# Performance work log

Hardware: AMD Instinct MI355X
Metric: run time of the kernel (lower is better)

## Reference

```python
import jax, jax.numpy as jnp
import numpy as np

# --- SLAYER params (nmnistNet.yaml) ---
THETA = 10.0
TS = 1.0
TAU_REF = 1.0
SCALE_REF = 2.0
T_SAMPLE = 300
B = 8

def _alpha_kernel(tau, mult, t_sample, ts, eps=0.01):
    vals = []
    t = 0.0
    while t < t_sample:
        v = mult * t / tau * np.exp(1.0 - t / tau)
        if abs(v) < eps and t > tau:
            break
        vals.append(v)
        t += ts
    return np.asarray(vals, np.float32)

# refractory kernel: alpha kernel with mult = -scaleRef*theta (slayer._calculateRefKernel)
REF_KERNEL = _alpha_kernel(TAU_REF, -SCALE_REF * THETA, T_SAMPLE, TS)
NREF = REF_KERNEL.shape[0]  # 11 for these params; REF_KERNEL[0] == 0


def spike(u):
    """slayerCuda.getSpikes: per-neuron sequential threshold recurrence over time.
    u: [..., T] membrane potential. On spike at t, REF_KERNEL is accumulated
    into u[t:t+NREF]; spike amplitude is 1/Ts."""
    uT = jnp.moveaxis(u, -1, 0)  # [T, ...]
    refk = jnp.asarray(REF_KERNEL[1:]).reshape((NREF - 1,) + (1,) * (u.ndim - 1))
    buf0 = jnp.zeros((NREF - 1,) + uT.shape[1:], u.dtype)  # pending refractory

    def step(buf, u_t):
        u_mod = u_t + buf[0]
        ev = (u_mod >= THETA).astype(u.dtype)
        buf = jnp.concatenate([buf[1:], jnp.zeros_like(buf[:1])], axis=0) + ev[None] * refk
        return buf, ev / TS

    _, s = jax.lax.scan(step, buf0, uT)
    return jnp.moveaxis(s, 0, -1)


def conv2d_t(x, w, pad):
    """slayer.conv: Conv3d with kernel (k,k,1) == per-timestep 2D conv.
    x: [B,C,H,W,T], w: [O,I,kh,kw]."""
    b, c, h, wd, t = x.shape
    xb = jnp.moveaxis(x, -1, 1).reshape(b * t, c, h, wd)
    y = jax.lax.conv_general_dilated(xb, w, (1, 1), [(pad, pad), (pad, pad)],
                                     dimension_numbers=('NCHW', 'OIHW', 'NCHW'))
    o, ho, wo = y.shape[1], y.shape[2], y.shape[3]
    return jnp.moveaxis(y.reshape(b, t, o, ho, wo), 1, -1)


def sum_pool2(x):
    """slayer.pool(2): fixed-weight (1.1*theta) 2x2/stride-2 sum over H,W per channel."""
    y = jax.lax.reduce_window(x, 0.0, jax.lax.add, (1, 1, 2, 2, 1), (1, 1, 2, 2, 1), 'VALID')
    return 1.1 * THETA * y


def setup_inputs():
    key = jax.random.key(0)
    k0, k1, k2, k3, k4 = jax.random.split(key, 5)
    spikeInput = (jax.random.uniform(k0, (B, 2, 34, 34, T_SAMPLE)) < 0.1).astype(jnp.float32) / TS
    # conv weights: kaiming-uniform bound * 100 (the __init__ scales conv weights by 100)
    w1 = jax.random.uniform(k1, (16, 2, 5, 5), minval=-14.1, maxval=14.1, dtype=jnp.float32)
    w2 = jax.random.uniform(k2, (32, 16, 3, 3), minval=-8.3, maxval=8.3, dtype=jnp.float32)
    w3 = jax.random.uniform(k3, (64, 32, 3, 3), minval=-5.9, maxval=5.9, dtype=jnp.float32)
    wfc = jax.random.uniform(k4, (10, 64, 8, 8), minval=-0.5, maxval=0.5, dtype=jnp.float32)
    return {"spikeInput": spikeInput, "w1": w1, "w2": w2, "w3": w3, "wfc": wfc}


def reference(spikeInput, w1, w2, w3, wfc):
    s1 = spike(conv2d_t(spikeInput, w1, 1))  # [B,16,32,32,T]
    s2 = spike(sum_pool2(s1))                # [B,16,16,16,T]
    s3 = spike(conv2d_t(s2, w2, 1))          # [B,32,16,16,T]
    s4 = spike(sum_pool2(s3))                # [B,32,8,8,T]
    s5 = spike(conv2d_t(s4, w3, 1))          # [B,64,8,8,T]
    # dense((8,8,64),10): Conv3d(64,10,(8,8,1)) == full-spatial contraction
    u = jnp.einsum('bchwt,ochw->bot', s5, wfc)[:, :, None, None, :]
    return spike(u)                          # [B,10,1,1,T]
```

## Files before the change

kernel.cpp:

```cpp
#include <hip/hip_runtime.h>
#include <hip/hip_bf16.h>
#include <cmath>

#define T_SAMPLE 300
#define NCHUNK 75

typedef __attribute__((ext_vector_type(8))) short short8;
typedef __attribute__((ext_vector_type(4))) float f32x4;

struct RefK { float v[10]; };

__device__ __forceinline__ unsigned char spike_step(float u, float* buf, const RefK& rk) {
    const float um = u + buf[0];
    const bool fire = um >= 10.0f;
    const float ev = fire ? 1.0f : 0.0f;
#pragma unroll
    for (int r = 0; r < 9; ++r) buf[r] = fmaf(ev, rk.v[r], buf[r + 1]);
    buf[9] = ev * rk.v[9];
    return fire ? (unsigned char)1 : (unsigned char)0;
}

__device__ __forceinline__ short8 bytes_to_bf16x8(uint2 w8) {
    union { uint4 u; short8 s8; } cv;
    cv.u.x = (w8.x & 0xFFu) * 0x3F80u | ((((w8.x >> 8) & 0xFFu) * 0x3F80u) << 16);
    cv.u.y = ((w8.x >> 16) & 0xFFu) * 0x3F80u | ((((w8.x >> 24) & 0xFFu) * 0x3F80u) << 16);
    cv.u.z = (w8.y & 0xFFu) * 0x3F80u | ((((w8.y >> 8) & 0xFFu) * 0x3F80u) << 16);
    cv.u.w = ((w8.y >> 16) & 0xFFu) * 0x3F80u | ((((w8.y >> 24) & 0xFFu) * 0x3F80u) << 16);
    return cv.s8;
}

__device__ __forceinline__ unsigned short bf16_split_sel(float w, int s) {
    __hip_bfloat16 hb = __float2bfloat16(w);
    const float hf = __bfloat162float(hb);
    __hip_bfloat16 mb = __float2bfloat16(w - hf);
    const float mf = __bfloat162float(mb);
    __hip_bfloat16 lb = __float2bfloat16(w - hf - mf);
    __hip_bfloat16 sel = (s == 0) ? hb : ((s == 1) ? mb : lb);
    return *(unsigned short*)&sel;
}

__global__ __launch_bounds__(256) void transpose_in_k(
    const float* __restrict__ In, unsigned int* __restrict__ X)
{
    __shared__ unsigned int lds[16 * NCHUNK];
    const int blk = blockIdx.x;
    const int tn = threadIdx.x >> 4;
    const int tq = threadIdx.x & 15;
    const size_t n = (size_t)blk * 16 + tn;
#pragma unroll
    for (int p = 0; p < 5; ++p) {
        const int ch = p * 16 + tq;
        if (ch < NCHUNK) {
            const float4 v = *(const float4*)(In + n * T_SAMPLE + ch * 4);
            unsigned int u = (v.x != 0.f ? 1u : 0u) | (v.y != 0.f ? 0x100u : 0u) |
                             (v.z != 0.f ? 0x10000u : 0u) | (v.w != 0.f ? 0x1000000u : 0u);
            lds[tn * NCHUNK + ch] = u;
        }
    }
    __syncthreads();
    for (int idx = threadIdx.x; idx < 16 * NCHUNK; idx += 256) {
        const int ch = idx >> 4, t2 = idx & 15;
        X[(size_t)ch * 18496 + blk * 16 + t2] = lds[t2 * NCHUNK + ch];
    }
}

__global__ __launch_bounds__(256) void prep_w1_k(
    const float* __restrict__ w1, unsigned short* __restrict__ Wr1)
{
    const int g = blockIdx.x * 256 + threadIdx.x;
    const int j = g & 7;
    const int lane = (g >> 3) & 63;
    const int ks = (g >> 9) & 3;
    const int s = g >> 11;
    const int q = lane >> 4;
    const int oc = lane & 15;
    const int kg = ks * 32 + q * 8 + j;
    const int slot = kg >> 2, c = kg & 1;
    const int dy = slot / 6, dx = slot % 6;
    const float w = (dy < 5 && dx < 5) ? w1[((oc * 2 + c) * 5 + dy) * 5 + dx] * 0.5f : 0.f;
    Wr1[g] = bf16_split_sel(w, s);
}

__global__ __launch_bounds__(256) void prep_w3_k(
    const float* __restrict__ w3, unsigned short* __restrict__ Wr)
{
    const int g = blockIdx.x * 256 + threadIdx.x;
    const int j = g & 7;
    const int lane = (g >> 3) & 63;
    const int mt = (g >> 9) & 3;
    const int rest = g >> 11;
    const int ks = rest % 9;
    const int s = rest / 9;
    const int oc = mt * 16 + (lane & 15);
    const int ic = (lane >> 4) * 8 + j;
    Wr[g] = bf16_split_sel(w3[(oc * 32 + ic) * 9 + ks], s);
}

__global__ __launch_bounds__(256) void prep_w2_k(
    const float* __restrict__ w2, unsigned short* __restrict__ Wr2)
{
    const int g = blockIdx.x * 256 + threadIdx.x;
    const int j = g & 7;
    const int lane = (g >> 3) & 63;
    const int mt = (g >> 9) & 1;
    const int rest = g >> 10;
    const int kp = rest % 5;
    const int s = rest / 5;
    const int q = lane >> 4;
    const int oc = mt * 16 + (lane & 15);
    const int tap = kp * 2 + (q >> 1);
    const int ic = (q & 1) * 8 + j;
    const float w = (tap <= 8) ? w2[(oc * 16 + ic) * 9 + tap] : 0.f;
    Wr2[g] = bf16_split_sel(w, s);
}

__device__ __forceinline__ void c1_mfma_chunk(
    const unsigned int* __restrict__ tb, const int* offA, const int* offB,
    const short8* Af, f32x4* acc)
{
    unsigned int vA[4][4], vB[4][4];
#pragma unroll
    for (int ks = 0; ks < 4; ++ks)
#pragma unroll
        for (int t = 0; t < 4; ++t) {
            vA[ks][t] = tb[t * 72 + offA[ks]];
            vB[ks][t] = tb[t * 72 + offB[ks]];
        }

#pragma unroll
    for (int t = 0; t < 4; ++t) acc[t] = (f32x4){0.f, 0.f, 0.f, 0.f};
#pragma unroll
    for (int ks = 0; ks < 4; ++ks)
#pragma unroll
        for (int t = 0; t < 4; ++t) {
            union { uint4 u; short8 s8; } cv;
            cv.u.x = vA[ks][t]; cv.u.y = vA[ks][t];
            cv.u.z = vB[ks][t]; cv.u.w = vB[ks][t];
#pragma unroll
            for (int s = 0; s < 3; ++s)
                acc[t] = __builtin_amdgcn_mfma_f32_16x16x32_bf16(
                    Af[s * 4 + ks], cv.s8, acc[t], 0, 0, 0);
        }
}

__global__ __launch_bounds__(512, 4) void conv1pc_k(
    const unsigned int* __restrict__ X, const unsigned short* __restrict__ Wr1,
    uchar4* __restrict__ S1, RefK rk)
{
    __shared__ unsigned int tab[2][4 * 288];
    __shared__ __align__(16) float4 Ulds[2][4 * 256];
    const int pg = blockIdx.x;
    const int b = blockIdx.y;
    const int ty = pg >> 2, tx = pg & 3;
    const int tid = threadIdx.x;
    const int wv = tid >> 6, lane = tid & 63;
    const bool isConv = (wv >= 4);
    const int q = lane >> 4, n = lane & 15;
    const int py0 = n >> 3, px0 = n & 7;

    short8 Af[12];
    int offA[4], offB[4];
    int lidx[2], gof[2];
    unsigned int w0[2], w1[2];
    if (isConv) {
#pragma unroll
        for (int s = 0; s < 3; ++s)
#pragma unroll
            for (int ks = 0; ks < 4; ++ks)
                Af[s * 4 + ks] = *(const short8*)(Wr1 + (((s * 4 + ks) * 64 + lane) * 8));
#pragma unroll
        for (int ks = 0; ks < 4; ++ks) {
            const int sA = ks * 8 + q * 2, sB = sA + 1;
            const int dyA = sA / 6, dxA = sA - dyA * 6;
            const int dyB = sB / 6, dxB = sB - dyB * 6;
            offA[ks] = min(py0 + dyA, 5) * 12 + min(px0 + dxA, 11);
            offB[ks] = min(py0 + dyB, 5) * 12 + min(px0 + dxB, 11);
        }
        const int tid2 = tid - 256;
#pragma unroll
        for (int i = 0; i < 2; ++i) {
            const int e = i * 256 + tid2;
            if (e < 288) {
                const int chl = e / 72, site = e - chl * 72;
                const int r = site / 12, cc = site - r * 12;
                const int gy = ty * 2 - 1 + r, gx = tx * 8 - 1 + cc;
                lidx[i] = chl * 288 + site;
                gof[i] = (((unsigned)gy < 34u) && ((unsigned)gx < 34u))
                       ? (chl * 18496 + (b * 2) * 1156 + gy * 34 + gx) : -1;
            } else { lidx[i] = -1; gof[i] = -1; }
        }
#pragma unroll
        for (int i = 0; i < 2; ++i) {
            if (gof[i] >= 0) { w0[i] = X[gof[i]]; w1[i] = X[gof[i] + 1156]; }
            else { w0[i] = 0u; w1[i] = 0u; }
        }
#pragma unroll
        for (int i = 0; i < 2; ++i) {
            if (lidx[i] >= 0) {
#pragma unroll
                for (int t = 0; t < 4; ++t)
                    tab[0][lidx[i] + t * 72] =
                        ((w0[i] >> (8 * t)) & 0xFFu) * 0x3F80u
                        | ((((w1[i] >> (8 * t)) & 0xFFu) * 0x3F80u) << 16);
            }
        }
    }

    float buf[10];
#pragma unroll
    for (int r = 0; r < 10; ++r) buf[r] = 0.f;
    const int s_oc = (tid & 255) >> 4, s_n = tid & 15;
    const int nb0 = (b * 16 + s_oc) * 1024 + (ty * 2 + (s_n >> 3)) * 32 + tx * 8 + (s_n & 7);

    __syncthreads();

    for (int w = 0; w < 19; ++w) {
        const int cb = w & 1;
        if (isConv) {
            if (w < 18) {
                const unsigned int* Xs = X + (size_t)(w + 1) * (4 * 18496);
#pragma unroll
                for (int i = 0; i < 2; ++i) {
                    if (gof[i] >= 0) { w0[i] = Xs[gof[i]]; w1[i] = Xs[gof[i] + 1156]; }
                }
            }
            const int CW = (w == 18) ? 3 : 4;
            const int k = wv - 4;
            if (k < CW) {
                f32x4 acc[4];
                c1_mfma_chunk(&tab[cb][k * 288], offA, offB, Af, acc);
#pragma unroll
                for (int rr = 0; rr < 4; ++rr)
                    Ulds[cb][k * 256 + (q * 4 + rr) * 16 + n] =
                        make_float4(acc[0][rr], acc[1][rr], acc[2][rr], acc[3][rr]);
            }
            if (w < 18) {
#pragma unroll
                for (int i = 0; i < 2; ++i) {
                    if (lidx[i] >= 0) {
#pragma unroll
                        for (int t = 0; t < 4; ++t)
                            tab[cb ^ 1][lidx[i] + t * 72] =
                                ((w0[i] >> (8 * t)) & 0xFFu) * 0x3F80u
                                | ((((w1[i] >> (8 * t)) & 0xFFu) * 0x3F80u) << 16);
                    }
                }
            }
        } else if (w > 0) {
            const int pb = (w - 1) & 1;
            for (int k = 0; k < 4; ++k) {
                const float4 u = Ulds[pb][k * 256 + tid];
                uchar4 o;
                o.x = spike_step(u.x, buf, rk);
                o.y = spike_step(u.y, buf, rk);
                o.z = spike_step(u.z, buf, rk);
                o.w = spike_step(u.w, buf, rk);
                S1[(size_t)((w - 1) * 4 + k) * 131072 + nb0] = o;
            }
        }
        __syncthreads();
    }
    if (!isConv) {
        for (int k = 0; k < 3; ++k) {
            const float4 u = Ulds[0][k * 256 + tid];
            uchar4 o;
            o.x = spike_step(u.x, buf, rk);
            o.y = spike_step(u.y, buf, rk);
            o.z = spike_step(u.z, buf, rk);
            o.w = spike_step(u.w, buf, rk);
            S1[(size_t)(72 + k) * 131072 + nb0] = o;
        }
    }
}

__global__ __launch_bounds__(256) void conv2_mfma_k(
    const unsigned int* __restrict__ s2u, const unsigned short* __restrict__ Wr2,
    float4* __restrict__ U, int b0, int nbl)
{
    __shared__ __align__(16) unsigned char pad[4 * 18 * 18 * 16];
    const int tc = blockIdx.x;
    const int bl = blockIdx.z;
    const int b = b0 + bl;
    const int tid = threadIdx.x;
    const int wv = tid >> 6, lane = tid & 63;
    const int q = lane >> 4, n = lane & 15;
    const int PLANE_U = nbl * 8192;

    unsigned int* lp = (unsigned int*)pad;
    for (int i = tid; i < 5184; i += 256) lp[i] = 0u;
    __syncthreads();
    const unsigned int* sb = s2u + (size_t)tc * 32768 + b * 4096;
    for (int e = tid; e < 4096; e += 256) {
        const unsigned int v = sb[e];
        const int c = e >> 8, pix = e & 255;
        const int base = (((pix >> 4) + 1) * 18 + ((pix & 15) + 1)) * 16 + c;
        pad[base]         = (unsigned char)(v & 0xFFu);
        pad[5184 + base]  = (unsigned char)((v >> 8) & 0xFFu);
        pad[10368 + base] = (unsigned char)((v >> 16) & 0xFFu);
        pad[15552 + base] = (unsigned char)(v >> 24);
    }
    __syncthreads();

    for (int i = 0; i < 4; ++i) {
        const int r = wv * 4 + i;
        f32x4 acc[2][4];
#pragma unroll
        for (int mt = 0; mt < 2; ++mt)
#pragma unroll
            for (int t = 0; t < 4; ++t) acc[mt][t] = (f32x4){0.f, 0.f, 0.f, 0.f};

        for (int kp = 0; kp < 5; ++kp) {
            short8 Af[6];
#pragma unroll
            for (int s = 0; s < 3; ++s)
#pragma unroll
                for (int mt = 0; mt < 2; ++mt)
                    Af[s * 2 + mt] = *(const short8*)(Wr2 + ((((s * 5 + kp) * 2 + mt) * 64 + lane) * 8));
            int tap = kp * 2 + (q >> 1);
            if (tap > 8) tap = 8;
            const int dy = tap / 3, dx = tap % 3;
#pragma unroll
            for (int t = 0; t < 4; ++t) {
                const int off = ((t * 18 + r + dy) * 18 + (n + dx)) * 16 + (q & 1) * 8;
                const short8 Bf = bytes_to_bf16x8(*(const uint2*)(pad + off));
#pragma unroll
                for (int s = 0; s < 3; ++s)
#pragma unroll
                    for (int mt = 0; mt < 2; ++mt)
                        acc[mt][t] = __builtin_amdgcn_mfma_f32_16x16x32_bf16(
                            Af[s * 2 + mt], Bf, acc[mt][t], 0, 0, 0);
            }
        }

        const size_t ub = (size_t)tc * PLANE_U;
#pragma unroll
        for (int mt = 0; mt < 2; ++mt)
#pragma unroll
            for (int rr = 0; rr < 4; ++rr) {
                const int oc = mt * 16 + q * 4 + rr;
                const int nb = (bl * 32 + oc) * 256 + r * 16 + n;
                U[ub + nb] = make_float4(acc[mt][0][rr], acc[mt][1][rr], acc[mt][2][rr], acc[mt][3][rr]);
            }
    }
}

__global__ __launch_bounds__(256) void conv3_mfma_k(
    const unsigned int* __restrict__ s4u, const unsigned short* __restrict__ Wr,
    float4* __restrict__ U)
{
    __shared__ __align__(16) unsigned char pad[12800];
    const int tc = blockIdx.x;
    const int bl = blockIdx.z;
    const int tid = threadIdx.x;
    const int wv = tid >> 6, lane = tid & 63;
    const int q = lane >> 4, n = lane & 15;

    unsigned int* lp = (unsigned int*)pad;
    for (int i = tid; i < 3200; i += 256) lp[i] = 0u;
    __syncthreads();
    const unsigned int* sb = s4u + (size_t)tc * 16384 + bl * 2048;
    for (int e = tid; e < 2048; e += 256) {
        const unsigned int v = sb[e];
        const int c = e >> 6, pix = e & 63;
        const int base = (((pix >> 3) + 1) * 10 + ((pix & 7) + 1)) * 32 + c;
        pad[base]        = (unsigned char)(v & 0xFFu);
        pad[3200 + base] = (unsigned char)((v >> 8) & 0xFFu);
        pad[6400 + base] = (unsigned char)((v >> 16) & 0xFFu);
        pad[9600 + base] = (unsigned char)(v >> 24);
    }
    __syncthreads();

    const int pixel = wv * 16 + n;
    const int py0 = pixel >> 3, px0 = pixel & 7;

    f32x4 acc[4][4];
#pragma unroll
    for (int mt = 0; mt < 4; ++mt)
#pragma unroll
        for (int t = 0; t < 4; ++t) acc[mt][t] = (f32x4){0.f, 0.f, 0.f, 0.f};

    for (int ks = 0; ks < 9; ++ks) {
        const int dy = ks / 3, dx = ks % 3;
        short8 Af[12];
#pragma unroll
        for (int s = 0; s < 3; ++s)
#pragma unroll
            for (int mt = 0; mt < 4; ++mt)
                Af[s * 4 + mt] = *(const short8*)(Wr + ((((s * 9 + ks) * 4 + mt) * 64 + lane) * 8));
#pragma unroll
        for (int t = 0; t < 4; ++t) {
            const int off = ((t * 10 + py0 + dy) * 10 + (px0 + dx)) * 32 + q * 8;
            const short8 Bf = bytes_to_bf16x8(*(const uint2*)(pad + off));
#pragma unroll
            for (int s = 0; s < 3; ++s)
#pragma unroll
                for (int mt = 0; mt < 4; ++mt)
                    acc[mt][t] = __builtin_amdgcn_mfma_f32_16x16x32_bf16(
                        Af[s * 4 + mt], Bf, acc[mt][t], 0, 0, 0);
        }
    }

    const size_t ub = (size_t)tc * 32768 + (size_t)bl * 4096;
#pragma unroll
    for (int mt = 0; mt < 4; ++mt)
#pragma unroll
        for (int r = 0; r < 4; ++r) {
            const int oc = mt * 16 + q * 4 + r;
            const int nb = oc * 64 + wv * 16 + n;
            U[ub + nb] = make_float4(acc[mt][0][r], acc[mt][1][r], acc[mt][2][r], acc[mt][3][r]);
        }
}

__device__ __forceinline__ void spike_body(
    const float4* __restrict__ U, uchar4* __restrict__ S,
    int nneur, int sstride, int soff, const RefK& rk)
{
    const int n = blockIdx.x * 64 + threadIdx.x;
    const float4* up = U + n;
    uchar4* sp = S + soff + n;
    float buf[10];
#pragma unroll
    for (int r = 0; r < 10; ++r) buf[r] = 0.f;

    float4 ring[8];
#pragma unroll
    for (int r = 0; r < 8; ++r) ring[r] = up[(size_t)r * nneur];

#pragma unroll 8
    for (int ch = 0; ch < 72; ++ch) {
        const float4 cur = ring[ch & 7];
        const int pf = (ch + 8 < NCHUNK) ? ch + 8 : NCHUNK - 1;
        ring[ch & 7] = up[(size_t)pf * nneur];
        uchar4 o;
        o.x = spike_step(cur.x, buf, rk);
        o.y = spike_step(cur.y, buf, rk);
        o.z = spike_step(cur.z, buf, rk);
        o.w = spike_step(cur.w, buf, rk);
        sp[(size_t)ch * sstride] = o;
    }
#pragma unroll
    for (int ch = 72; ch < NCHUNK; ++ch) {
        const float4 cur = ring[ch & 7];
        uchar4 o;
        o.x = spike_step(cur.x, buf, rk);
        o.y = spike_step(cur.y, buf, rk);
        o.z = spike_step(cur.z, buf, rk);
        o.w = spike_step(cur.w, buf, rk);
        sp[(size_t)ch * sstride] = o;
    }
}

__global__ __launch_bounds__(64) void spike2_k(
    const float4* U, uchar4* S, int nneur, int sstride, int soff, RefK rk)
{ spike_body(U, S, nneur, sstride, soff, rk); }

__global__ __launch_bounds__(64) void spike3_k(
    const float4* U, uchar4* S, int nneur, int sstride, int soff, RefK rk)
{ spike_body(U, S, nneur, sstride, soff, rk); }

__device__ __forceinline__ int bsum4(uint2 r0, uint2 r1, int k) {
    return (int)((r0.x >> (8 * k)) & 0xffu) + (int)((r0.y >> (8 * k)) & 0xffu)
         + (int)((r1.x >> (8 * k)) & 0xffu) + (int)((r1.y >> (8 * k)) & 0xffu);
}

template <int C, int H, int W>
__device__ __forceinline__ void pool_body(
    const uchar4* __restrict__ Sin, uchar4* __restrict__ Sout, const RefK& rk)
{
    constexpr int H2 = H / 2, W2 = W / 2;
    constexpr int SIN = 8 * C * H * W;
    constexpr int SOUT = 8 * C * H2 * W2;
    const int n = blockIdx.x * 64 + threadIdx.x;
    const int x = n % W2;
    const int y = (n / W2) % H2;
    const int c = (n / (W2 * H2)) % C;
    const int b = n / (W2 * H2 * C);
    const int base = (((b * C + c) * H + 2 * y) * W + 2 * x);
    uchar4* q = Sout + n;

    float buf[10];
#pragma unroll
    for (int r = 0; r < 10; ++r) buf[r] = 0.f;

    uint2 r0[8], r1[8];
#pragma unroll
    for (int r = 0; r < 8; ++r) {
        r0[r] = *(const uint2*)(Sin + (size_t)r * SIN + base);
        r1[r] = *(const uint2*)(Sin + (size_t)r * SIN + base + W);
    }

#pragma unroll 8
    for (int ch = 0; ch < 72; ++ch) {
        const uint2 a0 = r0[ch & 7], a1 = r1[ch & 7];
        const int pf = (ch + 8 < NCHUNK) ? ch + 8 : NCHUNK - 1;
        r0[ch & 7] = *(const uint2*)(Sin + (size_t)pf * SIN + base);
        r1[ch & 7] = *(const uint2*)(Sin + (size_t)pf * SIN + base + W);
        uchar4 o;
        o.x = spike_step(11.0f * (float)bsum4(a0, a1, 0), buf, rk);
        o.y = spike_step(11.0f * (float)bsum4(a0, a1, 1), buf, rk);
        o.z = spike_step(11.0f * (float)bsum4(a0, a1, 2), buf, rk);
        o.w = spike_step(11.0f * (float)bsum4(a0, a1, 3), buf, rk);
        q[(size_t)ch * SOUT] = o;
    }
#pragma unroll
    for (int ch = 72; ch < NCHUNK; ++ch) {
        const uint2 a0 = r0[ch & 7], a1 = r1[ch & 7];
        uchar4 o;
        o.x = spike_step(11.0f * (float)bsum4(a0, a1, 0), buf, rk);
        o.y = spike_step(11.0f * (float)bsum4(a0, a1, 1), buf, rk);
        o.z = spike_step(11.0f * (float)bsum4(a0, a1, 2), buf, rk);
        o.w = spike_step(11.0f * (float)bsum4(a0, a1, 3), buf, rk);
        q[(size_t)ch * SOUT] = o;
    }
}

__global__ __launch_bounds__(64) void pool2_k(
    const uchar4* Sin, uchar4* Sout, RefK rk) { pool_body<16, 32, 32>(Sin, Sout, rk); }
__global__ __launch_bounds__(64) void pool4_k(
    const uchar4* Sin, uchar4* Sout, RefK rk) { pool_body<32, 16, 16>(Sin, Sout, rk); }

__global__ __launch_bounds__(64) void dense_k(
    const uchar4* __restrict__ S5, const float* __restrict__ WFC,
    float4* __restrict__ U6)
{
    const int tc = blockIdx.x, o = blockIdx.y, b = blockIdx.z;
    const int lane = threadIdx.x;
    float a0 = 0.f, a1 = 0.f, a2 = 0.f, a3 = 0.f;
    const uchar4* sb = S5 + (size_t)tc * 32768 + b * 4096;
    const float* wb = WFC + o * 4096;
    for (int i = 0; i < 64; ++i) {
        const int site = i * 64 + lane;
        const uchar4 s = sb[site];
        const float w = wb[site];
        a0 = fmaf(w, (float)s.x, a0);
        a1 = fmaf(w, (float)s.y, a1);
        a2 = fmaf(w, (float)s.z, a2);
        a3 = fmaf(w, (float)s.w, a3);
    }
#pragma unroll
    for (int m = 1; m < 64; m <<= 1) {
        a0 += __shfl_xor(a0, m, 64);
        a1 += __shfl_xor(a1, m, 64);
        a2 += __shfl_xor(a2, m, 64);
        a3 += __shfl_xor(a3, m, 64);
    }
    if (lane == 0)
        U6[(size_t)tc * 80 + b * 10 + o] = make_float4(a0, a1, a2, a3);
}

__global__ __launch_bounds__(128) void spike6_k(
    const float4* __restrict__ U6, float* __restrict__ Out, RefK rk)
{
    const int n = threadIdx.x;
    if (n >= 80) return;
    const float4* up = U6 + n;
    float* op = Out + (size_t)n * T_SAMPLE;
    float buf[10];
#pragma unroll
    for (int r = 0; r < 10; ++r) buf[r] = 0.f;

    float4 ring[8];
#pragma unroll
    for (int r = 0; r < 8; ++r) ring[r] = up[(size_t)r * 80];

#pragma unroll 8
    for (int ch = 0; ch < 72; ++ch) {
        const float4 cur = ring[ch & 7];
        const int pf = (ch + 8 < NCHUNK) ? ch + 8 : NCHUNK - 1;
        ring[ch & 7] = up[(size_t)pf * 80];
        float4 o;
        o.x = (float)spike_step(cur.x, buf, rk);
        o.y = (float)spike_step(cur.y, buf, rk);
        o.z = (float)spike_step(cur.z, buf, rk);
        o.w = (float)spike_step(cur.w, buf, rk);
        *(float4*)(op + ch * 4) = o;
    }
#pragma unroll
    for (int ch = 72; ch < NCHUNK; ++ch) {
        const float4 cur = ring[ch & 7];
        float4 o;
        o.x = (float)spike_step(cur.x, buf, rk);
        o.y = (float)spike_step(cur.y, buf, rk);
        o.z = (float)spike_step(cur.z, buf, rk);
        o.w = (float)spike_step(cur.w, buf, rk);
        *(float4*)(op + ch * 4) = o;
    }
}

extern "C" void kernel_launch(void* const* d_in, const int* in_sizes, int n_in,
                              void* d_out, int out_size, void* d_ws, size_t ws_size,
                              hipStream_t stream)
{
    const float* spikeIn = (const float*)d_in[0];
    const float* w1 = (const float*)d_in[1];
    const float* w2 = (const float*)d_in[2];
    const float* w3 = (const float*)d_in[3];
    const float* wfc = (const float*)d_in[4];
    float* out = (float*)d_out;

    RefK rk;
    for (int t = 1; t <= 10; ++t)
        rk.v[t - 1] = (float)(-20.0 * (double)t * std::exp(1.0 - (double)t));

    const size_t A_BYTES = 39321600;
    const size_t B_BYTES = 9830400;
    const size_t U6_BYTES = 96000;
    const size_t U_BIG = 78643200, U_SMALL = 39321600;
    const size_t TAIL = A_BYTES + B_BYTES + U6_BYTES;
    const bool big = ws_size >= U_BIG + TAIL;
    const size_t U_BYTES = big ? U_BIG : U_SMALL;

    char* ws = (char*)d_ws;
    float4* U = (float4*)ws;
    uchar4* A = (uchar4*)(ws + U_BYTES);
    uchar4* Bb = (uchar4*)(ws + U_BYTES + A_BYTES);
    float4* U6 = (float4*)(ws + U_BYTES + A_BYTES + B_BYTES);
    unsigned short* Wr = (unsigned short*)(ws + U_BYTES + 20971520);
    unsigned short* Wr2 = (unsigned short*)(ws + U_BYTES + 20971520 + 131072);
    unsigned short* Wr1 = (unsigned short*)(ws + U_BYTES + A_BYTES + 5570560);

    uchar4* X = Bb;
    uchar4* s1 = A;
    uchar4* s2 = Bb;
    uchar4* s3 = A;
    uchar4* s4 = Bb;
    uchar4* s5 = A;

    transpose_in_k<<<18496 / 16, 256, 0, stream>>>(spikeIn, (unsigned int*)X);
    prep_w1_k<<<24, 256, 0, stream>>>(w1, Wr1);

    {
        dim3 g1(64, 8);
        conv1pc_k<<<g1, 512, 0, stream>>>((const unsigned int*)X, Wr1, s1, rk);
    }
    pool2_k<<<32768 / 64, 64, 0, stream>>>(s1, s2, rk);
    prep_w2_k<<<60, 256, 0, stream>>>(w2, Wr2);
    prep_w3_k<<<216, 256, 0, stream>>>(w3, Wr);
    const int nbl2 = big ? 8 : 4;
    for (int b0 = 0; b0 < 8; b0 += nbl2) {
        dim3 g2(NCHUNK, 1, nbl2);
        conv2_mfma_k<<<g2, 256, 0, stream>>>((const unsigned int*)s2, Wr2, U, b0, nbl2);
        const int nn = nbl2 * 8192;
        spike2_k<<<nn / 64, 64, 0, stream>>>(U, s3, nn, 65536, b0 * 8192, rk);
    }
    pool4_k<<<16384 / 64, 64, 0, stream>>>(s3, s4, rk);
    {
        dim3 g3(NCHUNK, 1, 8);
        conv3_mfma_k<<<g3, 256, 0, stream>>>((const unsigned int*)s4, Wr, U);
        spike3_k<<<32768 / 64, 64, 0, stream>>>(U, s5, 32768, 32768, 0, rk);
    }
    {
        dim3 g6(NCHUNK, 10, 8);
        dense_k<<<g6, 64, 0, stream>>>(s5, wfc, U6);
    }
    spike6_k<<<1, 128, 0, stream>>>(U6, out, rk);
}
```

Before: 249.4 us.

## Fuse first pooling-spike stage into conv1 kernel via shared-memory spike buffer

Adds a ninth wavefront to the conv1 block that consumes the layer-1 spikes from shared memory, does the 2x2 sum-pool and the second spike recurrence, and writes pooled spikes directly. This removes the global write and re-read of the full s1 tensor and the separate pool2 kernel launch. The pool runs one stage behind the spike wavefronts and adds an extra LDS buffer. The single pool wave does sequential work per chunk, which may lengthen the critical path, and dropping the (512,4) occupancy hint may lower occupancy.

```diff
diff --git a/kernel.cpp b/kernel.cpp
--- a/kernel.cpp
+++ b/kernel.cpp
@@ -143,18 +143,33 @@
         }
 }
 
-__global__ __launch_bounds__(512, 4) void conv1pc_k(
+__device__ __forceinline__ uchar4 pool_step4(
+    unsigned int g0, unsigned int g1, unsigned int g2, unsigned int g3,
+    float* buf2, const RefK& rk)
+{
+    uchar4 po;
+    po.x = spike_step(11.0f * (float)(((g0 >> 0) & 0xff) + ((g1 >> 0) & 0xff) + ((g2 >> 0) & 0xff) + ((g3 >> 0) & 0xff)), buf2, rk);
+    po.y = spike_step(11.0f * (float)(((g0 >> 8) & 0xff) + ((g1 >> 8) & 0xff) + ((g2 >> 8) & 0xff) + ((g3 >> 8) & 0xff)), buf2, rk);
+    po.z = spike_step(11.0f * (float)(((g0 >> 16) & 0xff) + ((g1 >> 16) & 0xff) + ((g2 >> 16) & 0xff) + ((g3 >> 16) & 0xff)), buf2, rk);
+    po.w = spike_step(11.0f * (float)(((g0 >> 24) & 0xff) + ((g1 >> 24) & 0xff) + ((g2 >> 24) & 0xff) + ((g3 >> 24) & 0xff)), buf2, rk);
+    return po;
+}
+
+__global__ __launch_bounds__(576) void conv1pc_k(
     const unsigned int* __restrict__ X, const unsigned short* __restrict__ Wr1,
-    uchar4* __restrict__ S1, RefK rk)
+    uchar4* __restrict__ S2, RefK rk)
 {
     __shared__ unsigned int tab[2][4 * 288];
     __shared__ __align__(16) float4 Ulds[2][4 * 256];
+    __shared__ unsigned int Sb[2][4 * 256];
     const int pg = blockIdx.x;
     const int b = blockIdx.y;
     const int ty = pg >> 2, tx = pg & 3;
     const int tid = threadIdx.x;
     const int wv = tid >> 6, lane = tid & 63;
-    const bool isConv = (wv >= 4);
+    const bool isConv = (wv >= 4 && wv < 8);
+    const bool isSpike = (wv < 4);
+    const bool isPool = (wv == 8);
     const int q = lane >> 4, n = lane & 15;
     const int py0 = n >> 3, px0 = n & 7;
 
@@ -209,8 +224,13 @@
     float buf[10];
 #pragma unroll
     for (int r = 0; r < 10; ++r) buf[r] = 0.f;
-    const int s_oc = (tid & 255) >> 4, s_n = tid & 15;
-    const int nb0 = (b * 16 + s_oc) * 1024 + (ty * 2 + (s_n >> 3)) * 32 + tx * 8 + (s_n & 7);
+
+    float buf2[10];
+#pragma unroll
+    for (int r = 0; r < 10; ++r) buf2[r] = 0.f;
+    const int oc_p = lane >> 2, xq = lane & 3;
+    const int src0 = oc_p * 16 + 2 * xq;
+    const size_t n2 = ((size_t)(b * 16 + oc_p) * 16 + ty) * 16 + tx * 4 + xq;
 
     __syncthreads();
 
@@ -246,29 +266,56 @@
                     }
                 }
             }
-        } else if (w > 0) {
+        } else if (isSpike && w > 0) {
             const int pb = (w - 1) & 1;
             for (int k = 0; k < 4; ++k) {
                 const float4 u = Ulds[pb][k * 256 + tid];
-                uchar4 o;
-                o.x = spike_step(u.x, buf, rk);
-                o.y = spike_step(u.y, buf, rk);
-                o.z = spike_step(u.z, buf, rk);
-                o.w = spike_step(u.w, buf, rk);
-                S1[(size_t)((w - 1) * 4 + k) * 131072 + nb0] = o;
+                union { uchar4 c; unsigned int i; } o;
+                o.c.x = spike_step(u.x, buf, rk);
+                o.c.y = spike_step(u.y, buf, rk);
+                o.c.z = spike_step(u.z, buf, rk);
+                o.c.w = spike_step(u.w, buf, rk);
+                Sb[pb][k * 256 + tid] = o.i;
             }
+        } else if (isPool && w >= 2) {
+            const int qb = (w - 2) & 1;
+            for (int k = 0; k < 4; ++k) {
+                const uchar4 po = pool_step4(
+                    Sb[qb][k * 256 + src0], Sb[qb][k * 256 + src0 + 1],
+                    Sb[qb][k * 256 + src0 + 8], Sb[qb][k * 256 + src0 + 9],
+                    buf2, rk);
+                S2[(size_t)((w - 2) * 4 + k) * 32768 + n2] = po;
+            }
         }
         __syncthreads();
     }
-    if (!isConv) {
+    if (isSpike) {
         for (int k = 0; k < 3; ++k) {
             const float4 u = Ulds[0][k * 256 + tid];
-            uchar4 o;
-            o.x = spike_step(u.x, buf, rk);
-            o.y = spike_step(u.y, buf, rk);
-            o.z = spike_step(u.z, buf, rk);
-            o.w = spike_step(u.w, buf, rk);
-            S1[(size_t)(72 + k) * 131072 + nb0] = o;
+            union { uchar4 c; unsigned int i; } o;
+            o.c.x = spike_step(u.x, buf, rk);
+            o.c.y = spike_step(u.y, buf, rk);
+            o.c.z = spike_step(u.z, buf, rk);
+            o.c.w = spike_step(u.w, buf, rk);
+            Sb[0][k * 256 + tid] = o.i;
+        }
+    } else if (isPool) {
+        for (int k = 0; k < 4; ++k) {
+            const uchar4 po = pool_step4(
+                Sb[1][k * 256 + src0], Sb[1][k * 256 + src0 + 1],
+                Sb[1][k * 256 + src0 + 8], Sb[1][k * 256 + src0 + 9],
+                buf2, rk);
+            S2[(size_t)(68 + k) * 32768 + n2] = po;
+        }
+    }
+    __syncthreads();
+    if (isPool) {
+        for (int k = 0; k < 3; ++k) {
+            const uchar4 po = pool_step4(
+                Sb[0][k * 256 + src0], Sb[0][k * 256 + src0 + 1],
+                Sb[0][k * 256 + src0 + 8], Sb[0][k * 256 + src0 + 9],
+                buf2, rk);
+            S2[(size_t)(72 + k) * 32768 + n2] = po;
         }
     }
 }
@@ -514,8 +561,6 @@
     }
 }
 
-__global__ __launch_bounds__(64) void pool2_k(
-    const uchar4* Sin, uchar4* Sout, RefK rk) { pool_body<16, 32, 32>(Sin, Sout, rk); }
 __global__ __launch_bounds__(64) void pool4_k(
     const uchar4* Sin, uchar4* Sout, RefK rk) { pool_body<32, 16, 16>(Sin, Sout, rk); }
 
@@ -612,28 +657,26 @@
 
     char* ws = (char*)d_ws;
     float4* U = (float4*)ws;
-    uchar4* A = (uchar4*)(ws + U_BYTES);
-    uchar4* Bb = (uchar4*)(ws + U_BYTES + A_BYTES);
+    char* Ab = ws + U_BYTES;
+    char* Bb = ws + U_BYTES + A_BYTES;
     float4* U6 = (float4*)(ws + U_BYTES + A_BYTES + B_BYTES);
-    unsigned short* Wr = (unsigned short*)(ws + U_BYTES + 20971520);
-    unsigned short* Wr2 = (unsigned short*)(ws + U_BYTES + 20971520 + 131072);
-    unsigned short* Wr1 = (unsigned short*)(ws + U_BYTES + A_BYTES + 5570560);
-
-    uchar4* X = Bb;
-    uchar4* s1 = A;
-    uchar4* s2 = Bb;
-    uchar4* s3 = A;
-    uchar4* s4 = Bb;
-    uchar4* s5 = A;
-
-    transpose_in_k<<<18496 / 16, 256, 0, stream>>>(spikeIn, (unsigned int*)X);
+    unsigned short* Wr = (unsigned short*)(Ab + 20971520);
+    unsigned short* Wr2 = (unsigned short*)(Ab + 20971520 + 131072);
+    unsigned short* Wr1 = (unsigned short*)(Bb + 5570560);
+
+    unsigned int* X = (unsigned int*)Bb;
+    uchar4* s2 = (uchar4*)(Ab + 25165824);
+    uchar4* s3 = (uchar4*)Ab;
+    uchar4* s4 = (uchar4*)Bb;
+    uchar4* s5 = (uchar4*)Ab;
+
+    transpose_in_k<<<18496 / 16, 256, 0, stream>>>(spikeIn, X);
     prep_w1_k<<<24, 256, 0, stream>>>(w1, Wr1);
 
     {
         dim3 g1(64, 8);
-        conv1pc_k<<<g1, 512, 0, stream>>>((const unsigned int*)X, Wr1, s1, rk);
-    }
-    pool2_k<<<32768 / 64, 64, 0, stream>>>(s1, s2, rk);
+        conv1pc_k<<<g1, 576, 0, stream>>>(X, Wr1, s2, rk);
+    }
     prep_w2_k<<<60, 256, 0, stream>>>(w2, Wr2);
     prep_w3_k<<<216, 256, 0, stream>>>(w3, Wr);
     const int nbl2 = big ? 8 : 4;
```

New measurement: 253.5 us. No clear change (+1.6%).

## Fuse second pooling layer into conv2 spike kernel via lane shuffles

Applied to the files above, without the earlier changes.

The spike kernel after conv2 now also performs the 2x2 sum-pool and the pool's spike recurrence. Each wavefront shuffles spike bytes from its 2x2 neighbours, and 16 lanes run the pooled recurrence and write s4 directly. This removes the pool4 launch and the round trip of the full s3 spike tensor through memory. In exchange it serialises extra recurrence work on a quarter of the lanes and adds four shuffles per time chunk. Workspace buffers are re-laid out to match.

```diff
diff --git a/kernel.cpp b/kernel.cpp
--- a/kernel.cpp
+++ b/kernel.cpp
@@ -18,6 +18,11 @@
     for (int r = 0; r < 9; ++r) buf[r] = fmaf(ev, rk.v[r], buf[r + 1]);
     buf[9] = ev * rk.v[9];
     return fire ? (unsigned char)1 : (unsigned char)0;
+}
+
+__device__ __forceinline__ int psum4(int g0, int g1, int g2, int g3, int sh) {
+    return ((g0 >> sh) & 0xff) + ((g1 >> sh) & 0xff)
+         + ((g2 >> sh) & 0xff) + ((g3 >> sh) & 0xff);
 }
 
 __device__ __forceinline__ short8 bytes_to_bf16x8(uint2 w8) {
@@ -411,9 +416,64 @@
         }
 }
 
-__device__ __forceinline__ void spike_body(
+__global__ __launch_bounds__(64) void spike2p_k(
+    const float4* __restrict__ U, uchar4* __restrict__ S4,
+    int nneur, int b0, RefK rk)
+{
+    const int lane = threadIdx.x;
+    const int n = blockIdx.x * 64 + lane;
+    const float4* up = U + n;
+    float buf[10], buf2[10];
+#pragma unroll
+    for (int r = 0; r < 10; ++r) { buf[r] = 0.f; buf2[r] = 0.f; }
+
+    const int bl = n >> 13, oc = (n >> 8) & 31, y = (n >> 4) & 15;
+    const int b = b0 + bl;
+    const int y0 = y & ~3;
+    const int p = lane & 15, ppy = p >> 3, ppx = p & 7;
+    const int sB = 32 * ppy + 2 * ppx;
+    const size_t s4base = (size_t)(b * 32 + oc) * 64 + ((y0 >> 1) + ppy) * 8 + ppx;
+
+    auto step_pool = [&](int ch, const float4& cur) {
+        union { uchar4 c; int i; } o;
+        o.c.x = spike_step(cur.x, buf, rk);
+        o.c.y = spike_step(cur.y, buf, rk);
+        o.c.z = spike_step(cur.z, buf, rk);
+        o.c.w = spike_step(cur.w, buf, rk);
+        const int g0 = __shfl(o.i, sB, 64);
+        const int g1 = __shfl(o.i, sB + 1, 64);
+        const int g2 = __shfl(o.i, sB + 16, 64);
+        const int g3 = __shfl(o.i, sB + 17, 64);
+        if (lane < 16) {
+            uchar4 po;
+            po.x = spike_step(11.0f * (float)psum4(g0, g1, g2, g3, 0), buf2, rk);
+            po.y = spike_step(11.0f * (float)psum4(g0, g1, g2, g3, 8), buf2, rk);
+            po.z = spike_step(11.0f * (float)psum4(g0, g1, g2, g3, 16), buf2, rk);
+            po.w = spike_step(11.0f * (float)psum4(g0, g1, g2, g3, 24), buf2, rk);
+            S4[(size_t)ch * 16384 + s4base] = po;
+        }
+    };
+
+    float4 ring[8];
+#pragma unroll
+    for (int r = 0; r < 8; ++r) ring[r] = up[(size_t)r * nneur];
+
+#pragma unroll 8
+    for (int ch = 0; ch < 72; ++ch) {
+        const float4 cur = ring[ch & 7];
+        const int pf = (ch + 8 < NCHUNK) ? ch + 8 : NCHUNK - 1;
+        ring[ch & 7] = up[(size_t)pf * nneur];
+        step_pool(ch, cur);
+    }
+#pragma unroll
+    for (int ch = 72; ch < NCHUNK; ++ch) {
+        step_pool(ch, ring[ch & 7]);
+    }
+}
+
+__global__ __launch_bounds__(64) void spike3_k(
     const float4* __restrict__ U, uchar4* __restrict__ S,
-    int nneur, int sstride, int soff, const RefK& rk)
+    int nneur, int sstride, int soff, RefK rk)
 {
     const int n = blockIdx.x * 64 + threadIdx.x;
     const float4* up = U + n;
@@ -449,14 +509,6 @@
         sp[(size_t)ch * sstride] = o;
     }
 }
-
-__global__ __launch_bounds__(64) void spike2_k(
-    const float4* U, uchar4* S, int nneur, int sstride, int soff, RefK rk)
-{ spike_body(U, S, nneur, sstride, soff, rk); }
-
-__global__ __launch_bounds__(64) void spike3_k(
-    const float4* U, uchar4* S, int nneur, int sstride, int soff, RefK rk)
-{ spike_body(U, S, nneur, sstride, soff, rk); }
 
 __device__ __forceinline__ int bsum4(uint2 r0, uint2 r1, int k) {
     return (int)((r0.x >> (8 * k)) & 0xffu) + (int)((r0.y >> (8 * k)) & 0xffu)
@@ -516,8 +568,6 @@
 
 __global__ __launch_bounds__(64) void pool2_k(
     const uchar4* Sin, uchar4* Sout, RefK rk) { pool_body<16, 32, 32>(Sin, Sout, rk); }
-__global__ __launch_bounds__(64) void pool4_k(
-    const uchar4* Sin, uchar4* Sout, RefK rk) { pool_body<32, 16, 16>(Sin, Sout, rk); }
 
 __global__ __launch_bounds__(64) void dense_k(
     const uchar4* __restrict__ S5, const float* __restrict__ WFC,
@@ -612,26 +662,24 @@
 
     char* ws = (char*)d_ws;
     float4* U = (float4*)ws;
-    uchar4* A = (uchar4*)(ws + U_BYTES);
-    uchar4* Bb = (uchar4*)(ws + U_BYTES + A_BYTES);
+    char* Ab = ws + U_BYTES;
+    char* Bb = ws + U_BYTES + A_BYTES;
     float4* U6 = (float4*)(ws + U_BYTES + A_BYTES + B_BYTES);
-    unsigned short* Wr = (unsigned short*)(ws + U_BYTES + 20971520);
-    unsigned short* Wr2 = (unsigned short*)(ws + U_BYTES + 20971520 + 131072);
-    unsigned short* Wr1 = (unsigned short*)(ws + U_BYTES + A_BYTES + 5570560);
-
-    uchar4* X = Bb;
-    uchar4* s1 = A;
-    uchar4* s2 = Bb;
-    uchar4* s3 = A;
-    uchar4* s4 = Bb;
-    uchar4* s5 = A;
-
-    transpose_in_k<<<18496 / 16, 256, 0, stream>>>(spikeIn, (unsigned int*)X);
+    unsigned short* Wr = (unsigned short*)(Ab + 20971520);
+    unsigned short* Wr2 = (unsigned short*)(Ab + 20971520 + 131072);
+    unsigned short* Wr1 = (unsigned short*)(Bb + 5570560);
+
+    unsigned int* X = (unsigned int*)Bb;
+    uchar4* s1 = (uchar4*)Ab;
+    uchar4* s2 = (uchar4*)Bb;
+    uchar4* s4 = (uchar4*)Ab;
+    uchar4* s5 = (uchar4*)(Ab + 5242880);
+    transpose_in_k<<<18496 / 16, 256, 0, stream>>>(spikeIn, X);
     prep_w1_k<<<24, 256, 0, stream>>>(w1, Wr1);
 
     {
         dim3 g1(64, 8);
-        conv1pc_k<<<g1, 512, 0, stream>>>((const unsigned int*)X, Wr1, s1, rk);
+        conv1pc_k<<<g1, 512, 0, stream>>>(X, Wr1, s1, rk);
     }
     pool2_k<<<32768 / 64, 64, 0, stream>>>(s1, s2, rk);
     prep_w2_k<<<60, 256, 0, stream>>>(w2, Wr2);
@@ -641,9 +689,8 @@
         dim3 g2(NCHUNK, 1, nbl2);
         conv2_mfma_k<<<g2, 256, 0, stream>>>((const unsigned int*)s2, Wr2, U, b0, nbl2);
         const int nn = nbl2 * 8192;
-        spike2_k<<<nn / 64, 64, 0, stream>>>(U, s3, nn, 65536, b0 * 8192, rk);
-    }
-    pool4_k<<<16384 / 64, 64, 0, stream>>>(s3, s4, rk);
+        spike2p_k<<<nn / 64, 64, 0, stream>>>(U, s4, nn, b0, rk);
+    }
     {
         dim3 g3(NCHUNK, 1, 8);
         conv3_mfma_k<<<g3, 256, 0, stream>>>((const unsigned int*)s4, Wr, U);
```

Result: no change. 252.1 us (+1.0%).
